# Kernel tuning notes

Measured on AMD Instinct MI355X. Metric: run time of the kernel, lower is better.

Reference implementation:

```python
import jax, jax.numpy as jnp
import numpy as np

H_DIM = 64
GRID = 8
NS = 2.0  # neighborhood_size


def _pool_seq(hidden, pos):
    # hidden: (P, H_DIM) hidden states of peds in one scene; pos: (P, 2) end positions
    P = hidden.shape[0]
    g2 = GRID * GRID
    tl_x = pos[:, 0] - NS / 2
    tl_y = pos[:, 1] + NS / 2
    br_x = pos[:, 0] + NS / 2
    br_y = pos[:, 1] - NS / 2
    # pair (i, j): grid of ped i (rows), position of ped j (cols)
    ox = pos[None, :, 0]
    oy = pos[None, :, 1]
    cell_x = jnp.floor((ox - tl_x[:, None]) / NS * GRID)
    cell_y = jnp.floor((tl_y[:, None] - oy) / NS * GRID)
    grid_pos = (cell_x + cell_y * GRID).astype(jnp.int32)
    # out-of-bound if outside neighborhood box OR i == j (diagonal forced out)
    oob = ((ox >= br_x[:, None]) | (ox <= tl_x[:, None])
           | (oy >= tl_y[:, None]) | (oy <= br_y[:, None])
           | jnp.eye(P, dtype=bool))
    idx = grid_pos + 1 + (jnp.arange(P, dtype=jnp.int32) * g2)[:, None]
    idx = jnp.where(oob, 0, idx)  # slot 0 is the trash bin (dropped below)
    src = jnp.broadcast_to(hidden[None], (P, P, H_DIM)).reshape(P * P, H_DIM)
    buf = jnp.zeros((P * g2 + 1, H_DIM), hidden.dtype)
    buf = buf.at[idx.reshape(-1)].add(src)
    return buf[1:].reshape(P, g2 * H_DIM)


def reference(h_states, seq_start_end, end_pos, rel_pos, W, b):
    B = end_pos.shape[0]
    S = seq_start_end.shape[0]
    P = B // S  # equal-length scenes -> static reshape
    hidden = h_states.reshape(-1, H_DIM).reshape(S, P, H_DIM)
    pos = end_pos.reshape(S, P, 2)
    pooled = jax.vmap(_pool_seq)(hidden, pos).reshape(B, GRID * GRID * H_DIM)
    # make_mlp([4096, 1024], relu, batch_norm=False): Linear -> ReLU
    return jax.nn.relu(pooled @ W + b)


def setup_inputs():
    key = jax.random.key(0)
    k0, k1, k2, k3 = jax.random.split(key, 4)
    S, P = 64, 64
    B = S * P
    bottleneck = 1024
    feat = GRID * GRID * H_DIM  # 4096
    h_states = jax.random.normal(k0, (1, B, H_DIM), jnp.float32)
    starts = jnp.arange(S, dtype=jnp.int32) * P
    seq_start_end = jnp.stack([starts, starts + P], axis=1)
    end_pos = jax.random.normal(k1, (B, 2), jnp.float32)
    rel_pos = jax.random.normal(k2, (B, 2), jnp.float32)
    W = jax.random.normal(k3, (feat, bottleneck), jnp.float32) * 0.02
    b = jnp.zeros((bottleneck,), jnp.float32)
    return {"h_states": h_states, "seq_start_end": seq_start_end,
            "end_pos": end_pos, "rel_pos": rel_pos, "W": W, "b": b}
```

## Files before the change

kernel.cpp:

```cpp
#include <hip/hip_runtime.h>


#define BM 128
#define BN 64
#define BK 128

typedef short short8 __attribute__((ext_vector_type(8)));
typedef short short4v __attribute__((ext_vector_type(4)));
typedef float floatx16 __attribute__((ext_vector_type(16)));

__device__ inline short f2bf(float x) {
    union { float f; unsigned u; } v; v.f = x;
    unsigned r = v.u + 0x7fffu + ((v.u >> 16) & 1u);
    return (short)(r >> 16);
}

__device__ inline void gload_lds16(const void* g, void* l) {
    __builtin_amdgcn_global_load_lds(
        (const __attribute__((address_space(1))) void*)g,
        (__attribute__((address_space(3))) void*)l,
        16, 0, 0);
}

__global__ __launch_bounds__(256) void prep_kernel(
    const float* __restrict__ h,
    const float* __restrict__ pos,
    short* __restrict__ pooled,
    const float* __restrict__ W,
    short* __restrict__ Wt,
    int K, int N, int poolBlocks)
{
    __shared__ __align__(16) unsigned char sh[18944];
    const int tid = threadIdx.x;

    if ((int)blockIdx.x < poolBlocks) {
        float* hs = (float*)sh;
        float* px = (float*)(sh + 16384);
        float* py = (float*)(sh + 16640);
        unsigned long long* wmask = (unsigned long long*)(sh + 16896);

        const int lane = tid & 63;
        const int w    = tid >> 6;
        const int s    = blockIdx.x >> 4;
        const int grp  = blockIdx.x & 15;
        const size_t base = (size_t)s * 64;

        const float4* hv  = (const float4*)(h + base * 64);
        float4*       hsv = (float4*)hs;
        #pragma unroll
        for (int c = 0; c < 4; ++c) hsv[tid + c * 256] = hv[tid + c * 256];
        if (tid < 64) {
            float2 p = ((const float2*)pos)[base + tid];
            px[tid] = p.x; py[tid] = p.y;
        }
        wmask[w * 64 + lane] = 0ull;
        __syncthreads();

        const int i = grp * 4 + w;
        const float tlx = px[i] - 1.0f;
        const float tly = py[i] + 1.0f;
        const float brx = px[i] + 1.0f;
        const float bry = py[i] - 1.0f;

        {
            const int j = lane;
            const float ox = px[j], oy = py[j];
            if (ox < brx && ox > tlx && oy < tly && oy > bry && j != i) {
                int cx = (int)floorf((ox - tlx) * 4.0f);
                int cy = (int)floorf((tly - oy) * 4.0f);
                atomicOr(&wmask[w * 64 + cx + cy * 8], 1ull << j);
            }
        }

        const int half = lane >> 5;
        const int d0   = (lane & 31) * 2;
        const size_t orow = (base + i) * 4096;
        unsigned short* pooledU = (unsigned short*)pooled;
        for (int c = 0; c < 64; c += 2) {
            unsigned long long m = wmask[w * 64 + c + half];
            float ax = 0.f, ay = 0.f;
            while (m) {
                int j0 = __builtin_ctzll(m); m &= m - 1;
                float2 hv2 = *(const float2*)&hs[j0 * 64 + d0];
                ax += hv2.x; ay += hv2.y;
            }
            unsigned pk = ((unsigned)(unsigned short)f2bf(ay) << 16)
                        |  (unsigned short)f2bf(ax);
            *(unsigned*)&pooledU[orow + (size_t)(c + half) * 64 + d0] = pk;
        }
    } else {
        float* t = (float*)sh;
        const int bid = blockIdx.x - poolBlocks;
        const int k0 = (bid & 63) * 64;
        const int n0 = (bid >> 6) * 64;

        const int r  = tid >> 4;
        const int cq = (tid & 15) * 4;
        #pragma unroll
        for (int i2 = 0; i2 < 4; ++i2) {
            const int row = r + i2 * 16;
            float4 v = *(const float4*)&W[(size_t)(k0 + row) * N + n0 + cq];
            t[row * 65 + cq + 0] = v.x; t[row * 65 + cq + 1] = v.y;
            t[row * 65 + cq + 2] = v.z; t[row * 65 + cq + 3] = v.w;
        }
        __syncthreads();
        const int nl = tid >> 4;
        const int kq = (tid & 15) * 4;
        #pragma unroll
        for (int i2 = 0; i2 < 4; ++i2) {
            const int n = nl + i2 * 16;
            short4v o;
            o.x = f2bf(t[(kq + 0) * 65 + n]); o.y = f2bf(t[(kq + 1) * 65 + n]);
            o.z = f2bf(t[(kq + 2) * 65 + n]); o.w = f2bf(t[(kq + 3) * 65 + n]);
            *(short4v*)&Wt[(size_t)(n0 + n) * K + k0 + kq] = o;
        }
    }
}

__global__ __launch_bounds__(256) void gemm_bias_relu(
    const short* __restrict__ A,
    const short* __restrict__ Bt,
    const float* __restrict__ bias,
    float* __restrict__ out,
    int M, int N, int K)
{
    __shared__ __align__(16) short As[BM * BK];
    __shared__ __align__(16) short Bs[BN * BK];

    const int tid  = threadIdx.x;
    const int lane = tid & 63;
    const int wave = tid >> 6;
    const int wr = wave >> 1;
    const int kh = wave & 1;
    const int nl = lane & 31;
    const int hl = lane >> 5;
    const int ml = lane & 15;

    const int b  = blockIdx.x;
    const int ib = b >> 3;
    const int m0 = ((b & 7) * 4 + (ib >> 4)) * BM;
    const int n0 = (ib & 15) * BN;

    const int r4   = lane >> 4;
    const int slot = lane & 15;

    const short* ag[8];
    const short* bg[4];
    #pragma unroll
    for (int c = 0; c < 8; ++c) {
        const int gi = c * 4 + wave;
        const int rl = gi * 4 + r4;
        ag[c] = A + (size_t)(m0 + rl) * K + (slot ^ (rl & 15)) * 8;
    }
    #pragma unroll
    for (int c = 0; c < 4; ++c) {
        const int gi = c * 4 + wave;
        const int rl = gi * 4 + r4;
        bg[c] = Bt + (size_t)(n0 + rl) * K + (slot ^ (rl & 15)) * 8;
    }

    floatx16 acc[4];
    #pragma unroll
    for (int i = 0; i < 4; ++i)
        #pragma unroll
        for (int r = 0; r < 16; ++r) acc[i][r] = 0.f;

    for (int kb = 0; kb < K; kb += BK) {
        if (kb) __syncthreads();
        #pragma unroll
        for (int c = 0; c < 8; ++c) {
            gload_lds16(ag[c], &As[(c * 4 + wave) * 512]);
            ag[c] += BK;
        }
        #pragma unroll
        for (int c = 0; c < 4; ++c) {
            gload_lds16(bg[c], &Bs[(c * 4 + wave) * 512]);
            bg[c] += BK;
        }
        __syncthreads();

        #pragma unroll
        for (int t = 0; t < 4; ++t) {
            const int g  = kh * 8 + 2 * t + hl;
            const int go = (g ^ ml) * 8;
            short8 a0 = *(const short8*)&As[(wr * 64 +      nl) * BK + go];
            short8 a1 = *(const short8*)&As[(wr * 64 + 32 + nl) * BK + go];
            short8 b0 = *(const short8*)&Bs[(          nl) * BK + go];
            short8 b1 = *(const short8*)&Bs[(     32 + nl) * BK + go];
            acc[0] = __builtin_amdgcn_mfma_f32_32x32x16_bf16(a0, b0, acc[0], 0, 0, 0);
            acc[1] = __builtin_amdgcn_mfma_f32_32x32x16_bf16(a0, b1, acc[1], 0, 0, 0);
            acc[2] = __builtin_amdgcn_mfma_f32_32x32x16_bf16(a1, b0, acc[2], 0, 0, 0);
            acc[3] = __builtin_amdgcn_mfma_f32_32x32x16_bf16(a1, b1, acc[3], 0, 0, 0);
        }
    }

    __syncthreads();
    float* red = (float*)As;
    if (kh) {
        #pragma unroll
        for (int mi = 0; mi < 2; ++mi)
            #pragma unroll
            for (int ni = 0; ni < 2; ++ni)
                #pragma unroll
                for (int r = 0; r < 16; ++r) {
                    const int row32 = (r & 3) + 8 * (r >> 2) + 4 * hl;
                    red[wr * 4096 + (mi * 32 + row32) * 64 + ni * 32 + nl] =
                        acc[mi * 2 + ni][r];
                }
    }
    __syncthreads();
    if (!kh) {
        const float bv0 = bias[n0 + nl];
        const float bv1 = bias[n0 + 32 + nl];
        #pragma unroll
        for (int mi = 0; mi < 2; ++mi)
            #pragma unroll
            for (int ni = 0; ni < 2; ++ni) {
                const float bv = ni ? bv1 : bv0;
                #pragma unroll
                for (int r = 0; r < 16; ++r) {
                    const int row32 = (r & 3) + 8 * (r >> 2) + 4 * hl;
                    const int gm = m0 + wr * 64 + mi * 32 + row32;
                    const int gn = n0 + ni * 32 + nl;
                    float v = acc[mi * 2 + ni][r]
                            + red[wr * 4096 + (mi * 32 + row32) * 64 + ni * 32 + nl]
                            + bv;
                    out[(size_t)gm * N + gn] = v > 0.f ? v : 0.f;
                }
            }
    }
}

extern "C" void kernel_launch(void* const* d_in, const int* in_sizes, int n_in,
                              void* d_out, int out_size, void* d_ws, size_t ws_size,
                              hipStream_t stream) {
    const float* h    = (const float*)d_in[0];
    const float* pos  = (const float*)d_in[2];
    const float* W    = (const float*)d_in[4];
    const float* bias = (const float*)d_in[5];

    const int B = in_sizes[0] / 64;
    const int N = in_sizes[5];
    const int K = 64 * 64;

    short* pooled = (short*)d_ws;
    short* Wt     = pooled + (size_t)B * K;
    float* out    = (float*)d_out;

    const int poolBlocks = B / 4;
    const int castBlocks = (K / 64) * (N / 64);
    prep_kernel<<<poolBlocks + castBlocks, 256, 0, stream>>>(
        h, pos, pooled, W, Wt, K, N, poolBlocks);
    gemm_bias_relu<<<(B / BM) * (N / BN), 256, 0, stream>>>(
        pooled, Wt, bias, out, B, N, K);
}
```

Before: 131.4 us.

## Double-buffer GEMM LDS tiles, widen N tile, and use 512-thread blocks

Widens the GEMM tile to 128x128 and uses 8 waves per block, split by M, N and K halves. Shared-memory A/B tiles become double-buffered so the next K slice's global-to-LDS loads are issued before the MFMAs on the current slice, with setprio raised around the MFMA loop. This aims to hide load latency and to reuse each A tile across more columns. In exchange it doubles LDS use to 128 KB per block and halves the grid to 256 blocks, which can lower occupancy and load balance across CUs.

```diff
diff --git a/kernel.cpp b/kernel.cpp
--- a/kernel.cpp
+++ b/kernel.cpp
@@ -2,7 +2,7 @@
 
 
 #define BM 128
-#define BN 64
+#define BN 128
 #define BK 128
 
 typedef short short8 __attribute__((ext_vector_type(8)));
@@ -117,45 +117,41 @@
     }
 }
 
-__global__ __launch_bounds__(256) void gemm_bias_relu(
+__global__ __launch_bounds__(512) void gemm_bias_relu(
     const short* __restrict__ A,
     const short* __restrict__ Bt,
     const float* __restrict__ bias,
     float* __restrict__ out,
     int M, int N, int K)
 {
-    __shared__ __align__(16) short As[BM * BK];
-    __shared__ __align__(16) short Bs[BN * BK];
+    __shared__ __align__(16) short As[2][BM * BK];
+    __shared__ __align__(16) short Bs[2][BN * BK];
 
     const int tid  = threadIdx.x;
     const int lane = tid & 63;
     const int wave = tid >> 6;
-    const int wr = wave >> 1;
     const int kh = wave & 1;
+    const int wn = (wave >> 1) & 1;
+    const int wr = wave >> 2;
     const int nl = lane & 31;
     const int hl = lane >> 5;
     const int ml = lane & 15;
 
     const int b  = blockIdx.x;
     const int ib = b >> 3;
-    const int m0 = ((b & 7) * 4 + (ib >> 4)) * BM;
-    const int n0 = (ib & 15) * BN;
+    const int m0 = ((b & 7) * 4 + (ib >> 3)) * BM;
+    const int n0 = (ib & 7) * BN;
 
     const int r4   = lane >> 4;
     const int slot = lane & 15;
 
-    const short* ag[8];
+    const short* ag[4];
     const short* bg[4];
     #pragma unroll
-    for (int c = 0; c < 8; ++c) {
-        const int gi = c * 4 + wave;
+    for (int c = 0; c < 4; ++c) {
+        const int gi = c * 8 + wave;
         const int rl = gi * 4 + r4;
-        ag[c] = A + (size_t)(m0 + rl) * K + (slot ^ (rl & 15)) * 8;
-    }
-    #pragma unroll
-    for (int c = 0; c < 4; ++c) {
-        const int gi = c * 4 + wave;
-        const int rl = gi * 4 + r4;
+        ag[c] = A  + (size_t)(m0 + rl) * K + (slot ^ (rl & 15)) * 8;
         bg[c] = Bt + (size_t)(n0 + rl) * K + (slot ^ (rl & 15)) * 8;
     }
 
@@ -165,36 +161,40 @@
         #pragma unroll
         for (int r = 0; r < 16; ++r) acc[i][r] = 0.f;
 
-    for (int kb = 0; kb < K; kb += BK) {
-        if (kb) __syncthreads();
-        #pragma unroll
-        for (int c = 0; c < 8; ++c) {
-            gload_lds16(ag[c], &As[(c * 4 + wave) * 512]);
-            ag[c] += BK;
-        }
-        #pragma unroll
-        for (int c = 0; c < 4; ++c) {
-            gload_lds16(bg[c], &Bs[(c * 4 + wave) * 512]);
-            bg[c] += BK;
-        }
-        __syncthreads();
-
+    #pragma unroll
+    for (int c = 0; c < 4; ++c) { gload_lds16(ag[c], &As[0][(c * 8 + wave) * 512]); ag[c] += BK; }
+    #pragma unroll
+    for (int c = 0; c < 4; ++c) { gload_lds16(bg[c], &Bs[0][(c * 8 + wave) * 512]); bg[c] += BK; }
+    __syncthreads();
+
+    const int NT = K / BK;
+    for (int i = 0; i < NT; ++i) {
+        const int cur = i & 1;
+        if (i + 1 < NT) {
+            const int nxt = cur ^ 1;
+            #pragma unroll
+            for (int c = 0; c < 4; ++c) { gload_lds16(ag[c], &As[nxt][(c * 8 + wave) * 512]); ag[c] += BK; }
+            #pragma unroll
+            for (int c = 0; c < 4; ++c) { gload_lds16(bg[c], &Bs[nxt][(c * 8 + wave) * 512]); bg[c] += BK; }
+        }
+        __builtin_amdgcn_s_setprio(1);
         #pragma unroll
         for (int t = 0; t < 4; ++t) {
             const int g  = kh * 8 + 2 * t + hl;
             const int go = (g ^ ml) * 8;
-            short8 a0 = *(const short8*)&As[(wr * 64 +      nl) * BK + go];
-            short8 a1 = *(const short8*)&As[(wr * 64 + 32 + nl) * BK + go];
-            short8 b0 = *(const short8*)&Bs[(          nl) * BK + go];
-            short8 b1 = *(const short8*)&Bs[(     32 + nl) * BK + go];
+            short8 a0 = *(const short8*)&As[cur][(wr * 64 +      nl) * BK + go];
+            short8 a1 = *(const short8*)&As[cur][(wr * 64 + 32 + nl) * BK + go];
+            short8 b0 = *(const short8*)&Bs[cur][(wn * 64 +      nl) * BK + go];
+            short8 b1 = *(const short8*)&Bs[cur][(wn * 64 + 32 + nl) * BK + go];
             acc[0] = __builtin_amdgcn_mfma_f32_32x32x16_bf16(a0, b0, acc[0], 0, 0, 0);
             acc[1] = __builtin_amdgcn_mfma_f32_32x32x16_bf16(a0, b1, acc[1], 0, 0, 0);
             acc[2] = __builtin_amdgcn_mfma_f32_32x32x16_bf16(a1, b0, acc[2], 0, 0, 0);
             acc[3] = __builtin_amdgcn_mfma_f32_32x32x16_bf16(a1, b1, acc[3], 0, 0, 0);
         }
-    }
-
-    __syncthreads();
+        __builtin_amdgcn_s_setprio(0);
+        __syncthreads();
+    }
+
     float* red = (float*)As;
     if (kh) {
         #pragma unroll
@@ -204,14 +204,14 @@
                 #pragma unroll
                 for (int r = 0; r < 16; ++r) {
                     const int row32 = (r & 3) + 8 * (r >> 2) + 4 * hl;
-                    red[wr * 4096 + (mi * 32 + row32) * 64 + ni * 32 + nl] =
+                    red[(wr * 2 + wn) * 4096 + (mi * 32 + row32) * 64 + ni * 32 + nl] =
                         acc[mi * 2 + ni][r];
                 }
     }
     __syncthreads();
     if (!kh) {
-        const float bv0 = bias[n0 + nl];
-        const float bv1 = bias[n0 + 32 + nl];
+        const float bv0 = bias[n0 + wn * 64 + nl];
+        const float bv1 = bias[n0 + wn * 64 + 32 + nl];
         #pragma unroll
         for (int mi = 0; mi < 2; ++mi)
             #pragma unroll
@@ -221,9 +221,9 @@
                 for (int r = 0; r < 16; ++r) {
                     const int row32 = (r & 3) + 8 * (r >> 2) + 4 * hl;
                     const int gm = m0 + wr * 64 + mi * 32 + row32;
-                    const int gn = n0 + ni * 32 + nl;
+                    const int gn = n0 + wn * 64 + ni * 32 + nl;
                     float v = acc[mi * 2 + ni][r]
-                            + red[wr * 4096 + (mi * 32 + row32) * 64 + ni * 32 + nl]
+                            + red[(wr * 2 + wn) * 4096 + (mi * 32 + row32) * 64 + ni * 32 + nl]
                             + bv;
                     out[(size_t)gm * N + gn] = v > 0.f ? v : 0.f;
                 }
@@ -251,6 +251,6 @@
     const int castBlocks = (K / 64) * (N / 64);
     prep_kernel<<<poolBlocks + castBlocks, 256, 0, stream>>>(
         h, pos, pooled, W, Wt, K, N, poolBlocks);
-    gemm_bias_relu<<<(B / BM) * (N / BN), 256, 0, stream>>>(
+    gemm_bias_relu<<<(B / BM) * (N / BN), 512, 0, stream>>>(
         pooled, Wt, bias, out, B, N, K);
 }
```

Measured after the change: 135.0 us. 2.7% more time.
